# Kernel optimization log

Hardware: AMD Instinct MI355X
Metric: run time of the kernel (lower is better)

Reference implementation:

```python
import jax, jax.numpy as jnp
import numpy as np

IN_C, H, W = 64, 256, 256
K = 3
OUT_C = 128


def setup_inputs() -> dict:
    key = jax.random.key(0)
    k1, k2 = jax.random.split(key)
    x = jax.random.normal(k1, (IN_C, H, W), dtype=jnp.float32)
    limit = np.sqrt(6.0 / (IN_C * K * K + OUT_C)).astype(np.float32)
    kernels = jax.random.uniform(k2, (OUT_C, IN_C, K, K), minval=-limit, maxval=limit, dtype=jnp.float32)
    biases = jnp.zeros((OUT_C,), dtype=jnp.float32)
    return {"x": x, "kernels": kernels, "biases": biases}


def reference(x, kernels, biases):
    # Cross-correlation (patch * kernel, no flip), VALID padding, CHW single image.
    out = jax.lax.conv_general_dilated(
        x[None],                      # [1, C, H, W]
        kernels,                      # [O, I, K, K]
        window_strides=(1, 1),
        padding="VALID",
        dimension_numbers=("NCHW", "OIHW", "NCHW"),
    )[0]                              # [O, H-K+1, W-K+1]
    return out + biases[:, None, None]
```

## Files before the change

### kernel.cpp

```cpp
#include <hip/hip_runtime.h>
#include <stdint.h>

#define IN_C 64
#define HH 256
#define WW 256
#define HW (HH * WW)
#define OUT_C 128
#define OH 254
#define OW 254
#define OHW (OH * OW)

#define XR 4
#define XW 66
#define CPAD 72

typedef __attribute__((ext_vector_type(4))) float f32x4;
typedef __attribute__((ext_vector_type(8))) __bf16 bf16x8;

__device__ __forceinline__ unsigned short f2bf(float f) {
  union { float f; unsigned u; } v; v.f = f;
  unsigned r = v.u + 0x7FFFu + ((v.u >> 16) & 1u);
  return (unsigned short)(r >> 16);
}

__global__ void prep_w(const float* __restrict__ w, unsigned short* __restrict__ wt) {
  const int idx = blockIdx.x * 256 + threadIdx.x;
  if (idx >= 9 * 8192) return;
  const int j    = idx & 7;
  const int lane = (idx >> 3) & 63;
  const int mt   = (idx >> 9) & 7;
  const int ch   = (idx >> 12) & 1;
  const int tap  = idx >> 13;
  const int o = mt * 16 + (lane & 15);
  const int c = ch * 32 + (lane >> 4) * 8 + j;
  wt[idx] = f2bf(w[(o * IN_C + c) * 9 + tap]);
}

__global__ __launch_bounds__(256, 3) void conv_mfma(
    const float* __restrict__ x, const unsigned short* __restrict__ wt,
    const float* __restrict__ bias, float* __restrict__ out) {
  __shared__ __align__(16) unsigned short Xs[XR * XW * CPAD];

  const int tid  = threadIdx.x;
  const int wave = tid >> 6;
  const int lane = tid & 63;
  const int x0 = blockIdx.x * 64;
  const int y0 = blockIdx.y * 2;

  const int mhalf = wave & 1;
  const int row   = wave >> 1;
  const int nlane = lane & 15;
  const int quad  = lane >> 4;

  const bf16x8* __restrict__ Wp = ((const bf16x8*)wt) + lane + (mhalf * 4) * 64;
  bf16x8 afA[4], afB[4];
#pragma unroll
  for (int mt = 0; mt < 4; ++mt) afA[mt] = Wp[mt * 64];

  {
    const int cq = tid & 15;
    const int xh = tid >> 4;

    int hc[2], hr[2], hx[2];
    float hv[2];
#pragma unroll
    for (int h = 0; h < 2; ++h) {
      const int k = tid + h * 256;
      hc[h] = k & 63;
      const int q = k >> 6;
      hx[h] = 64 + (q & 1);
      hr[h] = q >> 1;
      int xg = x0 + hx[h];
      if (xg > WW - 1) xg = WW - 1;
      hv[h] = x[hc[h] * HW + (y0 + hr[h]) * WW + xg];
    }

    f32x4 vv[4][4];
#pragma unroll
    for (int r = 0; r < 4; ++r) {
      const float* bx = x + (y0 + r) * WW + x0 + xh * 4;
#pragma unroll
      for (int cc = 0; cc < 4; ++cc)
        vv[r][cc] = *(const f32x4*)(bx + (cq * 4 + cc) * HW);
    }

#pragma unroll
    for (int r = 0; r < 4; ++r) {
#pragma unroll
      for (int xxi = 0; xxi < 4; ++xxi) {
        unsigned u0 = (unsigned)f2bf(vv[r][0][xxi]) | ((unsigned)f2bf(vv[r][1][xxi]) << 16);
        unsigned u1 = (unsigned)f2bf(vv[r][2][xxi]) | ((unsigned)f2bf(vv[r][3][xxi]) << 16);
        *(uint2*)&Xs[(r * XW + xh * 4 + xxi) * CPAD + cq * 4] = make_uint2(u0, u1);
      }
    }
#pragma unroll
    for (int h = 0; h < 2; ++h)
      Xs[(hr[h] * XW + hx[h]) * CPAD + hc[h]] = f2bf(hv[h]);
  }

  f32x4 acc[4][4];
#pragma unroll
  for (int mt = 0; mt < 4; ++mt) {
    const f32x4 bv = *(const f32x4*)(bias + (mhalf * 4 + mt) * 16 + quad * 4);
#pragma unroll
    for (int nt = 0; nt < 4; ++nt) acc[mt][nt] = bv;
  }

  __syncthreads();

#pragma unroll 1
  for (int pair = 0; pair < 9; ++pair) {
    const int ky = pair / 3;
    const int kx = pair - ky * 3;
    const int r = row + ky;
    const unsigned short* xrow = &Xs[(r * XW + kx) * CPAD + quad * 8];

#pragma unroll
    for (int mt = 0; mt < 4; ++mt) afB[mt] = Wp[((2 * pair + 1) * 8 + mt) * 64];

    {
      bf16x8 bfr[4];
#pragma unroll
      for (int nt = 0; nt < 4; ++nt)
        bfr[nt] = *(const bf16x8*)&xrow[(nt * 16 + nlane) * CPAD];
#pragma unroll
      for (int mt = 0; mt < 4; ++mt)
#pragma unroll
        for (int nt = 0; nt < 4; ++nt)
          acc[mt][nt] = __builtin_amdgcn_mfma_f32_16x16x32_bf16(afA[mt], bfr[nt], acc[mt][nt], 0, 0, 0);
    }

    if (pair < 8) {
#pragma unroll
      for (int mt = 0; mt < 4; ++mt) afA[mt] = Wp[((2 * pair + 2) * 8 + mt) * 64];
    }

    {
      bf16x8 bfr[4];
#pragma unroll
      for (int nt = 0; nt < 4; ++nt)
        bfr[nt] = *(const bf16x8*)&xrow[(nt * 16 + nlane) * CPAD + 32];
#pragma unroll
      for (int mt = 0; mt < 4; ++mt)
#pragma unroll
        for (int nt = 0; nt < 4; ++nt)
          acc[mt][nt] = __builtin_amdgcn_mfma_f32_16x16x32_bf16(afB[mt], bfr[nt], acc[mt][nt], 0, 0, 0);
    }
  }

  const int y = y0 + row;
#pragma unroll
  for (int mt = 0; mt < 4; ++mt) {
    const int obase = (mhalf * 4 + mt) * 16 + quad * 4;
#pragma unroll
    for (int nt = 0; nt < 4; ++nt) {
      const int xc = x0 + nt * 16 + nlane;
      if (xc < OW) {
        float* dst = out + obase * OHW + y * OW + xc;
#pragma unroll
        for (int reg = 0; reg < 4; ++reg)
          dst[reg * OHW] = acc[mt][nt][reg];
      }
    }
  }
}

extern "C" void kernel_launch(void* const* d_in, const int* in_sizes, int n_in,
                              void* d_out, int out_size, void* d_ws, size_t ws_size,
                              hipStream_t stream) {
  const float* x = (const float*)d_in[0];
  const float* w = (const float*)d_in[1];
  const float* b = (const float*)d_in[2];
  float* out = (float*)d_out;
  unsigned short* wt = (unsigned short*)d_ws;

  prep_w<<<dim3(288), dim3(256), 0, stream>>>(w, wt);
  conv_mfma<<<dim3(4, 127), dim3(256), 0, stream>>>(x, wt, b, out);
}
```

Baseline: 91.54 us.

## Pre-transpose input to bf16 channel-last layout and stream tiles via global_load_lds

Adds a prep kernel that converts x to bf16 in a pixel-major, channel-padded (HWC, 72-channel stride) layout. The weight repacking is folded into that same kernel. The conv kernel then fills its shared-memory tile with direct global-to-LDS 16-byte copies instead of doing strided fp32 loads, bf16 conversion and scattered LDS stores. This removes per-block conversion and transpose work and redundant fp32 reads, at the cost of an extra full pass over x plus a write of the transposed copy. The last tile reads slightly past the end of each row into padding or the next row, but only masked output columns depend on those values.

```diff
diff --git a/kernel.cpp b/kernel.cpp
--- a/kernel.cpp
+++ b/kernel.cpp
@@ -10,9 +10,9 @@
 #define OW 254
 #define OHW (OH * OW)
 
-#define XR 4
-#define XW 66
 #define CPAD 72
+#define XTROW (WW * CPAD)
+#define XSROW 5120
 
 typedef __attribute__((ext_vector_type(4))) float f32x4;
 typedef __attribute__((ext_vector_type(8))) __bf16 bf16x8;
@@ -23,23 +23,59 @@
   return (unsigned short)(r >> 16);
 }
 
-__global__ void prep_w(const float* __restrict__ w, unsigned short* __restrict__ wt) {
-  const int idx = blockIdx.x * 256 + threadIdx.x;
-  if (idx >= 9 * 8192) return;
-  const int j    = idx & 7;
-  const int lane = (idx >> 3) & 63;
-  const int mt   = (idx >> 9) & 7;
-  const int ch   = (idx >> 12) & 1;
-  const int tap  = idx >> 13;
-  const int o = mt * 16 + (lane & 15);
-  const int c = ch * 32 + (lane >> 4) * 8 + j;
-  wt[idx] = f2bf(w[(o * IN_C + c) * 9 + tap]);
+typedef const __attribute__((address_space(1))) unsigned GASU;
+typedef __attribute__((address_space(3))) unsigned LASU;
+__device__ __forceinline__ void gl_lds16(const void* g, void* l) {
+  __builtin_amdgcn_global_load_lds((GASU*)g, (LASU*)l, 16, 0, 0);
+}
+
+__global__ __launch_bounds__(256) void prep_x(
+    const float* __restrict__ x, const float* __restrict__ w,
+    unsigned short* __restrict__ xt, unsigned short* __restrict__ wt) {
+  __shared__ __align__(16) unsigned Ls[WW * 36];
+  const int y = blockIdx.x;
+  const int tid = threadIdx.x;
+  const int c2 = tid & 31;
+  const int g = tid >> 5;
+
+  const float* b0 = x + (2 * c2) * HW + y * WW + g * 32;
+  const float* b1 = b0 + HW;
+  f32x4 v0[8], v1[8];
+#pragma unroll
+  for (int i = 0; i < 8; ++i) v0[i] = *(const f32x4*)(b0 + i * 4);
+#pragma unroll
+  for (int i = 0; i < 8; ++i) v1[i] = *(const f32x4*)(b1 + i * 4);
+
+  for (int idx = blockIdx.x * 256 + tid; idx < 9 * 8192; idx += 65536) {
+    const int j = idx & 7;
+    const int ln = (idx >> 3) & 63;
+    const int mt = (idx >> 9) & 7;
+    const int ch = (idx >> 12) & 1;
+    const int tap = idx >> 13;
+    const int o = mt * 16 + (ln & 15);
+    const int c = ch * 32 + (ln >> 4) * 8 + j;
+    wt[idx] = f2bf(w[(o * IN_C + c) * 9 + tap]);
+  }
+
+#pragma unroll
+  for (int i = 0; i < 8; ++i)
+#pragma unroll
+    for (int j = 0; j < 4; ++j) {
+      const int px = g * 32 + i * 4 + j;
+      Ls[px * 36 + c2] = (unsigned)f2bf(v0[i][j]) | ((unsigned)f2bf(v1[i][j]) << 16);
+    }
+  __syncthreads();
+
+  uint4* dst = (uint4*)(xt + y * XTROW);
+  const uint4* src = (const uint4*)Ls;
+#pragma unroll
+  for (int k = 0; k < 9; ++k) dst[tid + k * 256] = src[tid + k * 256];
 }
 
 __global__ __launch_bounds__(256, 3) void conv_mfma(
-    const float* __restrict__ x, const unsigned short* __restrict__ wt,
+    const unsigned short* __restrict__ xt, const unsigned short* __restrict__ wt,
     const float* __restrict__ bias, float* __restrict__ out) {
-  __shared__ __align__(16) unsigned short Xs[XR * XW * CPAD];
+  __shared__ __align__(16) unsigned short Xs[4 * XSROW];
 
   const int tid  = threadIdx.x;
   const int wave = tid >> 6;
@@ -52,51 +88,18 @@
   const int nlane = lane & 15;
   const int quad  = lane >> 4;
 
+  {
+    const char* gsrc = (const char*)(xt + (y0 + wave) * XTROW + x0 * CPAD);
+    char* ldst = (char*)&Xs[wave * XSROW];
+#pragma unroll
+    for (int k = 0; k < 10; ++k)
+      gl_lds16(gsrc + k * 1024 + lane * 16, ldst + k * 1024);
+  }
+
   const bf16x8* __restrict__ Wp = ((const bf16x8*)wt) + lane + (mhalf * 4) * 64;
   bf16x8 afA[4], afB[4];
 #pragma unroll
   for (int mt = 0; mt < 4; ++mt) afA[mt] = Wp[mt * 64];
-
-  {
-    const int cq = tid & 15;
-    const int xh = tid >> 4;
-
-    int hc[2], hr[2], hx[2];
-    float hv[2];
-#pragma unroll
-    for (int h = 0; h < 2; ++h) {
-      const int k = tid + h * 256;
-      hc[h] = k & 63;
-      const int q = k >> 6;
-      hx[h] = 64 + (q & 1);
-      hr[h] = q >> 1;
-      int xg = x0 + hx[h];
-      if (xg > WW - 1) xg = WW - 1;
-      hv[h] = x[hc[h] * HW + (y0 + hr[h]) * WW + xg];
-    }
-
-    f32x4 vv[4][4];
-#pragma unroll
-    for (int r = 0; r < 4; ++r) {
-      const float* bx = x + (y0 + r) * WW + x0 + xh * 4;
-#pragma unroll
-      for (int cc = 0; cc < 4; ++cc)
-        vv[r][cc] = *(const f32x4*)(bx + (cq * 4 + cc) * HW);
-    }
-
-#pragma unroll
-    for (int r = 0; r < 4; ++r) {
-#pragma unroll
-      for (int xxi = 0; xxi < 4; ++xxi) {
-        unsigned u0 = (unsigned)f2bf(vv[r][0][xxi]) | ((unsigned)f2bf(vv[r][1][xxi]) << 16);
-        unsigned u1 = (unsigned)f2bf(vv[r][2][xxi]) | ((unsigned)f2bf(vv[r][3][xxi]) << 16);
-        *(uint2*)&Xs[(r * XW + xh * 4 + xxi) * CPAD + cq * 4] = make_uint2(u0, u1);
-      }
-    }
-#pragma unroll
-    for (int h = 0; h < 2; ++h)
-      Xs[(hr[h] * XW + hx[h]) * CPAD + hc[h]] = f2bf(hv[h]);
-  }
 
   f32x4 acc[4][4];
 #pragma unroll
@@ -113,7 +116,7 @@
     const int ky = pair / 3;
     const int kx = pair - ky * 3;
     const int r = row + ky;
-    const unsigned short* xrow = &Xs[(r * XW + kx) * CPAD + quad * 8];
+    const unsigned short* xrow = &Xs[r * XSROW + kx * CPAD + quad * 8];
 
 #pragma unroll
     for (int mt = 0; mt < 4; ++mt) afB[mt] = Wp[((2 * pair + 1) * 8 + mt) * 64];
@@ -173,7 +176,8 @@
   const float* b = (const float*)d_in[2];
   float* out = (float*)d_out;
   unsigned short* wt = (unsigned short*)d_ws;
+  unsigned short* xtb = (unsigned short*)((char*)d_ws + 262144);
 
-  prep_w<<<dim3(288), dim3(256), 0, stream>>>(w, wt);
-  conv_mfma<<<dim3(4, 127), dim3(256), 0, stream>>>(x, wt, b, out);
+  prep_x<<<dim3(256), dim3(256), 0, stream>>>(x, w, xtb, wt);
+  conv_mfma<<<dim3(4, 127), dim3(256), 0, stream>>>(xtb, wt, b, out);
 }
```

After: 92.38 us. No clear change (+0.9%).
